# Optimization experiments

Measured on AMD Instinct MI355X. Metric: run time of the kernel, lower is better.

## Reference

```python
import jax, jax.numpy as jnp
import numpy as np

ALPHA = 0.9
EPS = 1e-5
SEQ, BATCH, D_MODEL, FF_DIM = 2048, 16, 512, 2048


def _layer_norm(x, g, b):
    m = jnp.mean(x, axis=-1, keepdims=True)
    v = jnp.mean((x - m) ** 2, axis=-1, keepdims=True)
    return (x - m) * jax.lax.rsqrt(v + EPS) * g + b


def _decay_matrix(seq, dtype):
    # Closed form of the torch roll/flip/tril loop:
    #   W[i, j] = alpha^{i-j+1}            for j <= i
    #   W[i, i] += 1 - sum_{k=1}^{i+1} alpha^k   (diag correction)
    i = jnp.arange(seq)
    diff = i[:, None] - i[None, :]                       # [S, S]
    causal = diff >= 0
    expo = jnp.where(causal, diff + 1, 0).astype(dtype)
    W = jnp.where(causal, jnp.asarray(ALPHA, dtype) ** expo, 0.0)
    W = W + jnp.diag(1.0 - W.sum(axis=1))
    return W


def setup_inputs() -> dict:
    key = jax.random.key(0)
    ks = jax.random.split(key, 8)
    s = lambda fan: 1.0 / np.sqrt(fan)
    return {
        "x": jax.random.normal(ks[0], (SEQ, BATCH, D_MODEL), jnp.float32),
        "w_lin": jax.random.normal(ks[1], (D_MODEL, D_MODEL), jnp.float32) * s(D_MODEL),
        "b_lin": jax.random.normal(ks[2], (D_MODEL,), jnp.float32) * 0.01,
        "w1": jax.random.normal(ks[3], (FF_DIM, D_MODEL), jnp.float32) * s(D_MODEL),
        "b1": jax.random.normal(ks[4], (FF_DIM,), jnp.float32) * 0.01,
        "w2": jax.random.normal(ks[5], (D_MODEL, FF_DIM), jnp.float32) * s(FF_DIM),
        "b2": jax.random.normal(ks[6], (D_MODEL,), jnp.float32) * 0.01,
        "g1": jnp.ones((D_MODEL,), jnp.float32),
        "beta1": jnp.zeros((D_MODEL,), jnp.float32),
        "g2": jnp.ones((D_MODEL,), jnp.float32),
        "beta2": jnp.zeros((D_MODEL,), jnp.float32),
    }


def reference(x, w_lin, b_lin, w1, b1, w2, b2, g1, beta1, g2, beta2):
    seq = x.shape[0]
    W = _decay_matrix(seq, x.dtype)                      # [S, S]

    # attention sublayer (dropout = identity in eval)
    y = _layer_norm(x, g1, beta1)
    z = jnp.einsum("sbd,ed->sbe", y, w_lin) + b_lin       # projection
    attn = jnp.einsum("ih,hbd->ibd", W, z)                # causal exp-decay mixing
    x = x + attn

    # feed-forward sublayer
    y = _layer_norm(x, g2, beta2)
    h = jax.nn.relu(jnp.einsum("sbd,fd->sbf", y, w1) + b1)
    ff = jnp.einsum("sbf,df->sbd", h, w2) + b2
    return x + ff
```

## Files before the change

kernel.cpp:

```cpp
#include <hip/hip_runtime.h>

#define SEQ 2048
#define BATCH 16
#define DMODEL 512
#define FFDIM 2048
#define NTOK (SEQ * BATCH)
#define ALPHA 0.9f

typedef unsigned short u16;
typedef unsigned int u32;
typedef __attribute__((ext_vector_type(8))) short short8;
typedef __attribute__((ext_vector_type(4))) float f32x4;

__device__ __forceinline__ float bf2f(u16 u) {
    unsigned int v = ((unsigned int)u) << 16;
    return __builtin_bit_cast(float, v);
}
__device__ __forceinline__ u16 f2bf(float f) {
    unsigned int v = __builtin_bit_cast(unsigned int, f);
    v += 0x7fffu + ((v >> 16) & 1u);
    return (u16)(v >> 16);
}

__global__ __launch_bounds__(256) void cvt_kernel(const float* __restrict__ in,
                                                  u16* __restrict__ out, int n) {
    const int i = (blockIdx.x * 256 + threadIdx.x) * 4;
    if (i >= n) return;
    float4 v = *(const float4*)(in + i);
    ushort4 o;
    o.x = f2bf(v.x); o.y = f2bf(v.y); o.z = f2bf(v.z); o.w = f2bf(v.w);
    *(ushort4*)(out + i) = o;
}

__global__ __launch_bounds__(256) void ln_kernel(const float* __restrict__ xin,
                                                 const float* __restrict__ g,
                                                 const float* __restrict__ b,
                                                 u16* __restrict__ y) {
    const int lane = threadIdx.x & 63;
    const int wave = threadIdx.x >> 6;
    const long tok = (long)blockIdx.x * 4 + wave;
    const long off = tok * DMODEL + lane * 8;

    float f[8];
    {
        const float4* xp = (const float4*)(xin + off);
        float4 a = xp[0], c = xp[1];
        f[0] = a.x; f[1] = a.y; f[2] = a.z; f[3] = a.w;
        f[4] = c.x; f[5] = c.y; f[6] = c.z; f[7] = c.w;
    }
    float s = 0.f, s2 = 0.f;
#pragma unroll
    for (int i = 0; i < 8; i++) { s += f[i]; s2 += f[i] * f[i]; }
#pragma unroll
    for (int o = 32; o > 0; o >>= 1) {
        s += __shfl_xor(s, o, 64);
        s2 += __shfl_xor(s2, o, 64);
    }
    const float mean = s * (1.f / DMODEL);
    const float var = s2 * (1.f / DMODEL) - mean * mean;
    const float inv = rsqrtf(var + 1e-5f);

    const float4* gp = (const float4*)(g + lane * 8);
    const float4* bp = (const float4*)(b + lane * 8);
    float4 g0 = gp[0], g1 = gp[1], b0 = bp[0], b1 = bp[1];
    float gg[8] = {g0.x, g0.y, g0.z, g0.w, g1.x, g1.y, g1.z, g1.w};
    float bb[8] = {b0.x, b0.y, b0.z, b0.w, b1.x, b1.y, b1.z, b1.w};
    short8 ov;
#pragma unroll
    for (int i = 0; i < 8; i++)
        ov[i] = (short)f2bf((f[i] - mean) * inv * gg[i] + bb[i]);
    *(short8*)(y + off) = ov;
}

#define SCAN_L 64
#define NCHUNK (SEQ / SCAN_L)
#define NCOLU (BATCH * DMODEL / 2)
#define A64 1.17901846e-3f

__global__ __launch_bounds__(256) void wsum_kernel(const u16* __restrict__ z,
                                                   float* __restrict__ W) {
    const int colu = blockIdx.x * 256 + threadIdx.x;
    const int c = blockIdx.y;
    const int sb = c * SCAN_L;
    const u32* zp = (const u32*)z;

    float w0 = 0.f, w1 = 0.f;
    u32 zq[4];
#pragma unroll
    for (int j = 0; j < 4; j++) zq[j] = zp[(long)(sb + j) * NCOLU + colu];
#pragma unroll 4
    for (int i = 0; i < SCAN_L; i++) {
        const int sl = i & 3;
        const u32 zz = zq[sl];
        if (i + 4 < SCAN_L) zq[sl] = zp[(long)(sb + i + 4) * NCOLU + colu];
        w0 = ALPHA * (bf2f((u16)(zz & 0xffffu)) + w0);
        w1 = ALPHA * (bf2f((u16)(zz >> 16)) + w1);
    }
    ((float2*)W)[(long)c * NCOLU + colu] = (float2){w0, w1};
}

__global__ __launch_bounds__(256) void carry_kernel(const float* __restrict__ W,
                                                    float* __restrict__ R) {
    const int col = blockIdx.x * 256 + threadIdx.x;
    float r = 0.f;
#pragma unroll
    for (int c = 0; c < NCHUNK; c++) {
        R[(long)c * 8192 + col] = r;
        r = A64 * r + W[(long)c * 8192 + col];
    }
}

__global__ __launch_bounds__(256) void scan_kernel(const u16* __restrict__ z,
                                                   const float* __restrict__ x,
                                                   const float* __restrict__ Rbuf,
                                                   float* __restrict__ x1) {
    const int colu = blockIdx.x * 256 + threadIdx.x;
    const int c = blockIdx.y;
    const int s0 = c * SCAN_L;

    const u32* zp = (const u32*)z;
    const float2* xp = (const float2*)x;
    float2* x1p = (float2*)x1;

    const float2 rr = ((const float2*)Rbuf)[(long)c * NCOLU + colu];
    float r0 = rr.x, r1 = rr.y;

    float ap = powf(ALPHA, (float)(s0 + 2));

    u32 zq[4];
    float2 xq[4];
#pragma unroll
    for (int j = 0; j < 4; j++) {
        zq[j] = zp[(long)(s0 + j) * NCOLU + colu];
        xq[j] = xp[(long)(s0 + j) * NCOLU + colu];
    }
#pragma unroll 4
    for (int i = 0; i < SCAN_L; i++) {
        const int sl = i & 3;
        const u32 zz = zq[sl];
        const float2 xx = xq[sl];
        if (i + 4 < SCAN_L) {
            zq[sl] = zp[(long)(s0 + i + 4) * NCOLU + colu];
            xq[sl] = xp[(long)(s0 + i + 4) * NCOLU + colu];
        }
        const float z0 = bf2f((u16)(zz & 0xffffu));
        const float z1 = bf2f((u16)(zz >> 16));
        r0 = ALPHA * (z0 + r0);
        r1 = ALPHA * (z1 + r1);
        const float cc = 1.f - (ALPHA - ap) * 10.f;
        ap *= ALPHA;
        x1p[(long)(s0 + i) * NCOLU + colu] = (float2){xx.x + r0 + cc * z0, xx.y + r1 + cc * z1};
    }
}

#define BM 256
#define BN 256
#define BKK 64

typedef __attribute__((address_space(1))) unsigned int as1_u32;
typedef __attribute__((address_space(3))) unsigned int as3_u32;

__device__ __forceinline__ void gld_lds16(const void* g, const void* l) {
    __builtin_amdgcn_global_load_lds((as1_u32*)(unsigned long long)g,
                                     (as3_u32*)(unsigned int)(unsigned long long)l,
                                     16, 0, 0);
}

template <int EPI, bool OUT_F32>
__global__ __launch_bounds__(512, 2) void gemm8p(const u16* __restrict__ A,
                                                 const u16* __restrict__ Bt,
                                                 const float* __restrict__ bias,
                                                 const float* __restrict__ resid,
                                                 void* __restrict__ C,
                                                 int M, int N, int K) {
    __shared__ alignas(16) u16 sA[2][2][256 * 32];
    __shared__ alignas(16) u16 sB[2][2][256 * 32];

    const int tid = threadIdx.x;
    const int lane = tid & 63;
    const int wave = tid >> 6;
    const int wr = wave >> 2;
    const int wc = wave & 3;
    const int l15 = lane & 15, q16 = lane >> 4;

    const int gy = gridDim.y;
    const int nwg = gridDim.x * gy;
    const int d = blockIdx.y * gridDim.x + blockIdx.x;
    const int wgid = (d & 7) * (nwg >> 3) + (d >> 3);
    const int m0 = (wgid / gy) * BM;
    const int n0 = (wgid % gy) * BN;

    const u16* gA[2];
    const u16* gB[2];
    int dsto[2];
#pragma unroll
    for (int j = 0; j < 2; j++) {
        const int o = tid + j * 512;
        const int r = o >> 2;
        const int c = (o & 3) ^ ((o >> 3) & 3);
        gA[j] = A + (long)(m0 + r) * K + c * 8;
        gB[j] = Bt + (long)(n0 + r) * K + c * 8;
        dsto[j] = o * 8;
    }

    const int xoct = (q16 ^ ((l15 >> 1) & 3)) * 8;
    const int rowA = wr * 128 + l15;
    const int rowB = wc * 64 + l15;

    f32x4 acc[8][4];
#pragma unroll
    for (int i = 0; i < 8; i++)
#pragma unroll
        for (int j = 0; j < 4; j++) acc[i][j] = (f32x4){0.f, 0.f, 0.f, 0.f};

    const int NT = K / BKK;

#define STG_A(bs, kh, koff)                                                 \
    {                                                                       \
        gld_lds16(gA[0] + (koff) + (kh) * 32, &sA[bs][kh][dsto[0]]);        \
        gld_lds16(gA[1] + (koff) + (kh) * 32, &sA[bs][kh][dsto[1]]);        \
    }
#define STG_B(bs, kh, koff)                                                 \
    {                                                                       \
        gld_lds16(gB[0] + (koff) + (kh) * 32, &sB[bs][kh][dsto[0]]);        \
        gld_lds16(gB[1] + (koff) + (kh) * 32, &sB[bs][kh][dsto[1]]);        \
    }
#define MFMA16(mh)                                                          \
    {                                                                       \
        __builtin_amdgcn_s_setprio(1);                                      \
        _Pragma("unroll") for (int mi = 0; mi < 4; mi++)                    \
            _Pragma("unroll") for (int nj = 0; nj < 4; nj++)                \
                acc[(mh)*4 + mi][nj] = __builtin_amdgcn_mfma_f32_16x16x32_bf16( \
                    af[mi], bf[nj], acc[(mh)*4 + mi][nj], 0, 0, 0);         \
        __builtin_amdgcn_s_setprio(0);                                      \
    }
#define PHASE_END                                                           \
    {                                                                       \
        __builtin_amdgcn_sched_barrier(0);                                  \
        __builtin_amdgcn_s_barrier();                                       \
    }

    STG_A(0, 0, 0); STG_B(0, 0, 0); STG_A(0, 1, 0); STG_B(0, 1, 0);
    asm volatile("s_waitcnt vmcnt(4)" ::: "memory");
    __builtin_amdgcn_s_barrier();

#pragma unroll 1
    for (int t = 0; t < NT; ++t) {
        const int b = t & 1, bn = b ^ 1;
        const int ko = (t + 1) * BKK;
        const bool nx = (t + 1 < NT);
        short8 af[4], bf[4];

#pragma unroll
        for (int nj = 0; nj < 4; nj++)
            bf[nj] = *(const short8*)(&sB[b][0][(rowB + nj * 16) * 32 + xoct]);
#pragma unroll
        for (int mi = 0; mi < 4; mi++)
            af[mi] = *(const short8*)(&sA[b][0][(rowA + mi * 16) * 32 + xoct]);
        if (nx) STG_A(bn, 0, ko);
        MFMA16(0);
        PHASE_END;

#pragma unroll
        for (int mi = 0; mi < 4; mi++)
            af[mi] = *(const short8*)(&sA[b][0][(rowA + 64 + mi * 16) * 32 + xoct]);
        if (nx) STG_B(bn, 0, ko);
        MFMA16(1);
        if (nx) asm volatile("s_waitcnt vmcnt(4)" ::: "memory");
        else    asm volatile("s_waitcnt vmcnt(0)" ::: "memory");
        PHASE_END;

#pragma unroll
        for (int nj = 0; nj < 4; nj++)
            bf[nj] = *(const short8*)(&sB[b][1][(rowB + nj * 16) * 32 + xoct]);
#pragma unroll
        for (int mi = 0; mi < 4; mi++)
            af[mi] = *(const short8*)(&sA[b][1][(rowA + mi * 16) * 32 + xoct]);
        if (nx) STG_A(bn, 1, ko);
        MFMA16(0);
        PHASE_END;

#pragma unroll
        for (int mi = 0; mi < 4; mi++)
            af[mi] = *(const short8*)(&sA[b][1][(rowA + 64 + mi * 16) * 32 + xoct]);
        if (nx) STG_B(bn, 1, ko);
        MFMA16(1);
        if (nx) asm volatile("s_waitcnt vmcnt(4)" ::: "memory");
        else    asm volatile("s_waitcnt vmcnt(0)" ::: "memory");
        PHASE_END;
    }

#pragma unroll
    for (int mf = 0; mf < 8; mf++) {
        const int row0 = m0 + wr * 128 + mf * 16 + q16 * 4;
#pragma unroll
        for (int nj = 0; nj < 4; nj++) {
            const int col = n0 + wc * 64 + nj * 16 + l15;
            const float bv = bias[col];
#pragma unroll
            for (int r = 0; r < 4; r++) {
                const long idx = (long)(row0 + r) * N + col;
                float v = acc[mf][nj][r] + bv;
                if (EPI == 1) v = fmaxf(v, 0.f);
                if (EPI == 2) v += resid[idx];
                if (OUT_F32)
                    ((float*)C)[idx] = v;
                else
                    ((u16*)C)[idx] = f2bf(v);
            }
        }
    }
#undef STG_A
#undef STG_B
#undef MFMA16
#undef PHASE_END
}

extern "C" void kernel_launch(void* const* d_in, const int* in_sizes, int n_in,
                              void* d_out, int out_size, void* d_ws, size_t ws_size,
                              hipStream_t stream) {
    const float* x = (const float*)d_in[0];
    const float* w_lin = (const float*)d_in[1];
    const float* b_lin = (const float*)d_in[2];
    const float* w1 = (const float*)d_in[3];
    const float* b1 = (const float*)d_in[4];
    const float* w2 = (const float*)d_in[5];
    const float* b2 = (const float*)d_in[6];
    const float* g1 = (const float*)d_in[7];
    const float* be1 = (const float*)d_in[8];
    const float* g2 = (const float*)d_in[9];
    const float* be2 = (const float*)d_in[10];
    float* out = (float*)d_out;

    char* ws = (char*)d_ws;
    const size_t MB = 1024 * 1024;
    u16* y = (u16*)(ws);
    float* x1 = (float*)(ws + 32 * MB);
    u16* h = (u16*)(ws + 96 * MB);
    u16* z = h;
    float* Wbuf = (float*)(ws + 160 * MB);
    float* Rbuf = (float*)(ws + 162 * MB);
    u16* wb_lin = (u16*)(ws + 224 * MB);
    u16* wb1 = (u16*)(ws + 225 * MB);
    u16* wb2 = (u16*)(ws + 228 * MB);

    cvt_kernel<<<(DMODEL * DMODEL) / 1024, 256, 0, stream>>>(w_lin, wb_lin, DMODEL * DMODEL);
    cvt_kernel<<<(FFDIM * DMODEL) / 1024, 256, 0, stream>>>(w1, wb1, FFDIM * DMODEL);
    cvt_kernel<<<(DMODEL * FFDIM) / 1024, 256, 0, stream>>>(w2, wb2, DMODEL * FFDIM);

    ln_kernel<<<NTOK / 4, 256, 0, stream>>>(x, g1, be1, y);
    gemm8p<0, false><<<dim3(NTOK / BM, DMODEL / BN), 512, 0, stream>>>(y, wb_lin, b_lin, nullptr,
                                                                      z, NTOK, DMODEL, DMODEL);
    wsum_kernel<<<dim3(NCOLU / 256, NCHUNK), 256, 0, stream>>>(z, Wbuf);
    carry_kernel<<<8192 / 256, 256, 0, stream>>>(Wbuf, Rbuf);
    scan_kernel<<<dim3(NCOLU / 256, NCHUNK), 256, 0, stream>>>(z, x, Rbuf, x1);
    ln_kernel<<<NTOK / 4, 256, 0, stream>>>(x1, g2, be2, y);
    gemm8p<1, false><<<dim3(NTOK / BM, FFDIM / BN), 512, 0, stream>>>(y, wb1, b1, nullptr, h,
                                                                     NTOK, FFDIM, DMODEL);
    gemm8p<2, true><<<dim3(NTOK / BM, DMODEL / BN), 512, 0, stream>>>(h, wb2, b2, x1, out,
                                                                     NTOK, DMODEL, FFDIM);
}
```

Measured before the change: 421.1 us.

## Fuse second layernorm into decay scan and drop carry and extra convert launches

The scan kernel now has each block cover one batch item's full d_model row. It computes per-row LayerNorm statistics with wave shuffles and LDS during the scan, then re-reads its freshly written x1 tile to emit normalized bf16 y. The separate carry kernel is replaced by a truncated sum over the four previous chunk sums weighted by powers of alpha^chunk_len, and the three weight-convert launches are merged into one. This removes a full pass of the second LayerNorm and two launches. In exchange it adds per-row shuffle reductions inside the scan loop and a small approximation from dropping carries older than four chunks.

```diff
diff --git a/kernel.cpp b/kernel.cpp
--- a/kernel.cpp
+++ b/kernel.cpp
@@ -22,14 +22,20 @@
     return (u16)(v >> 16);
 }
 
-__global__ __launch_bounds__(256) void cvt_kernel(const float* __restrict__ in,
-                                                  u16* __restrict__ out, int n) {
+__global__ __launch_bounds__(256) void cvt3_kernel(const float* __restrict__ a, u16* __restrict__ da, int na,
+                                                   const float* __restrict__ b, u16* __restrict__ db, int nb,
+                                                   const float* __restrict__ c, u16* __restrict__ dc, int nc) {
     const int i = (blockIdx.x * 256 + threadIdx.x) * 4;
-    if (i >= n) return;
-    float4 v = *(const float4*)(in + i);
+    const float* s;
+    u16* d;
+    if (i < na) { s = a + i; d = da + i; }
+    else if (i < na + nb) { s = b + (i - na); d = db + (i - na); }
+    else if (i < na + nb + nc) { s = c + (i - na - nb); d = dc + (i - na - nb); }
+    else return;
+    float4 v = *(const float4*)s;
     ushort4 o;
     o.x = f2bf(v.x); o.y = f2bf(v.y); o.z = f2bf(v.z); o.w = f2bf(v.w);
-    *(ushort4*)(out + i) = o;
+    *(ushort4*)d = o;
 }
 
 __global__ __launch_bounds__(256) void ln_kernel(const float* __restrict__ xin,
@@ -99,31 +105,46 @@
     ((float2*)W)[(long)c * NCOLU + colu] = (float2){w0, w1};
 }
 
-__global__ __launch_bounds__(256) void carry_kernel(const float* __restrict__ W,
-                                                    float* __restrict__ R) {
-    const int col = blockIdx.x * 256 + threadIdx.x;
-    float r = 0.f;
-#pragma unroll
-    for (int c = 0; c < NCHUNK; c++) {
-        R[(long)c * 8192 + col] = r;
-        r = A64 * r + W[(long)c * 8192 + col];
-    }
-}
-
-__global__ __launch_bounds__(256) void scan_kernel(const u16* __restrict__ z,
-                                                   const float* __restrict__ x,
-                                                   const float* __restrict__ Rbuf,
-                                                   float* __restrict__ x1) {
-    const int colu = blockIdx.x * 256 + threadIdx.x;
+__global__ __launch_bounds__(256) void scanln_kernel(const u16* __restrict__ z,
+                                                     const float* __restrict__ x,
+                                                     const float* __restrict__ Wb,
+                                                     const float* __restrict__ g,
+                                                     const float* __restrict__ be,
+                                                     float* __restrict__ x1,
+                                                     u16* __restrict__ y) {
+    __shared__ float red[SCAN_L][4][2];
+    __shared__ float st[SCAN_L][2];
+
+    const int tid = threadIdx.x;
+    const int lane = tid & 63, wave = tid >> 6;
+    const int bx = blockIdx.x;
     const int c = blockIdx.y;
+    const int colu = bx * 256 + tid;
     const int s0 = c * SCAN_L;
 
     const u32* zp = (const u32*)z;
     const float2* xp = (const float2*)x;
     float2* x1p = (float2*)x1;
-
-    const float2 rr = ((const float2*)Rbuf)[(long)c * NCOLU + colu];
-    float r0 = rr.x, r1 = rr.y;
+    u32* yp = (u32*)y;
+    const float2* Wp = (const float2*)Wb;
+
+    const int d0 = 2 * tid;
+    const float gg0 = g[d0], gg1 = g[d0 + 1];
+    const float bb0 = be[d0], bb1 = be[d0 + 1];
+
+    float r0 = 0.f, r1 = 0.f;
+    {
+        float ak = 1.f;
+#pragma unroll
+        for (int k = 1; k <= 4; k++) {
+            if (c - k >= 0) {
+                const float2 w = Wp[(long)(c - k) * NCOLU + colu];
+                r0 += ak * w.x;
+                r1 += ak * w.y;
+            }
+            ak *= A64;
+        }
+    }
 
     float ap = powf(ALPHA, (float)(s0 + 2));
 
@@ -149,7 +170,45 @@
         r1 = ALPHA * (z1 + r1);
         const float cc = 1.f - (ALPHA - ap) * 10.f;
         ap *= ALPHA;
-        x1p[(long)(s0 + i) * NCOLU + colu] = (float2){xx.x + r0 + cc * z0, xx.y + r1 + cc * z1};
+        const float v0 = xx.x + r0 + cc * z0;
+        const float v1 = xx.y + r1 + cc * z1;
+        x1p[(long)(s0 + i) * NCOLU + colu] = (float2){v0, v1};
+
+        float s1 = v0 + v1, s2 = v0 * v0 + v1 * v1;
+#pragma unroll
+        for (int o = 32; o > 0; o >>= 1) {
+            s1 += __shfl_xor(s1, o, 64);
+            s2 += __shfl_xor(s2, o, 64);
+        }
+        if (lane == 0) {
+            red[i][wave][0] = s1;
+            red[i][wave][1] = s2;
+        }
+    }
+    __syncthreads();
+
+    if (tid < SCAN_L) {
+        const float S = red[tid][0][0] + red[tid][1][0] + red[tid][2][0] + red[tid][3][0];
+        const float S2 = red[tid][0][1] + red[tid][1][1] + red[tid][2][1] + red[tid][3][1];
+        const float mean = S * (1.f / DMODEL);
+        const float var = S2 * (1.f / DMODEL) - mean * mean;
+        st[tid][0] = mean;
+        st[tid][1] = rsqrtf(var + 1e-5f);
+    }
+    __syncthreads();
+
+    float2 vq[4];
+#pragma unroll
+    for (int j = 0; j < 4; j++) vq[j] = x1p[(long)(s0 + j) * NCOLU + colu];
+#pragma unroll 4
+    for (int i = 0; i < SCAN_L; i++) {
+        const int sl = i & 3;
+        const float2 v = vq[sl];
+        if (i + 4 < SCAN_L) vq[sl] = x1p[(long)(s0 + i + 4) * NCOLU + colu];
+        const float mean = st[i][0], inv = st[i][1];
+        const u16 o0 = f2bf((v.x - mean) * inv * gg0 + bb0);
+        const u16 o1 = f2bf((v.y - mean) * inv * gg1 + bb1);
+        yp[(long)(s0 + i) * NCOLU + colu] = ((u32)o1 << 16) | (u32)o0;
     }
 }
 
@@ -339,22 +398,19 @@
     u16* h = (u16*)(ws + 96 * MB);
     u16* z = h;
     float* Wbuf = (float*)(ws + 160 * MB);
-    float* Rbuf = (float*)(ws + 162 * MB);
     u16* wb_lin = (u16*)(ws + 224 * MB);
     u16* wb1 = (u16*)(ws + 225 * MB);
     u16* wb2 = (u16*)(ws + 228 * MB);
 
-    cvt_kernel<<<(DMODEL * DMODEL) / 1024, 256, 0, stream>>>(w_lin, wb_lin, DMODEL * DMODEL);
-    cvt_kernel<<<(FFDIM * DMODEL) / 1024, 256, 0, stream>>>(w1, wb1, FFDIM * DMODEL);
-    cvt_kernel<<<(DMODEL * FFDIM) / 1024, 256, 0, stream>>>(w2, wb2, DMODEL * FFDIM);
-
+    const int NA = DMODEL * DMODEL, NB = FFDIM * DMODEL, NC = DMODEL * FFDIM;
+
+    cvt3_kernel<<<(NA + NB + NC) / 1024, 256, 0, stream>>>(w_lin, wb_lin, NA,
+                                                           w1, wb1, NB, w2, wb2, NC);
     ln_kernel<<<NTOK / 4, 256, 0, stream>>>(x, g1, be1, y);
     gemm8p<0, false><<<dim3(NTOK / BM, DMODEL / BN), 512, 0, stream>>>(y, wb_lin, b_lin, nullptr,
                                                                       z, NTOK, DMODEL, DMODEL);
     wsum_kernel<<<dim3(NCOLU / 256, NCHUNK), 256, 0, stream>>>(z, Wbuf);
-    carry_kernel<<<8192 / 256, 256, 0, stream>>>(Wbuf, Rbuf);
-    scan_kernel<<<dim3(NCOLU / 256, NCHUNK), 256, 0, stream>>>(z, x, Rbuf, x1);
-    ln_kernel<<<NTOK / 4, 256, 0, stream>>>(x1, g2, be2, y);
+    scanln_kernel<<<dim3(BATCH, NCHUNK), 256, 0, stream>>>(z, x, Wbuf, g2, be2, x1, y);
     gemm8p<1, false><<<dim3(NTOK / BM, FFDIM / BN), 512, 0, stream>>>(y, wb1, b1, nullptr, h,
                                                                      NTOK, FFDIM, DMODEL);
     gemm8p<2, true><<<dim3(NTOK / BM, DMODEL / BN), 512, 0, stream>>>(h, wb2, b2, x1, out,
```

Measured after the change: 417.4 us. About the same (-0.9%).
